# Performance work log

Measured on AMD Instinct MI355X. Metric: run time of the kernel, lower is better.

The kernel has to match this reference:

```python
import jax, jax.numpy as jnp
import numpy as np

DN = ('NCHW', 'OIHW', 'NCHW')

def conv2d(x, w, b, stride, pad):
    y = jax.lax.conv_general_dilated(x, w, (stride, stride), [(pad, pad), (pad, pad)], dimension_numbers=DN)
    return y + b[None, :, None, None]

def conv_transpose2d(x, w, b):
    # torch ConvTranspose2d(k=4, stride=2, padding=1): out = (H-1)*2 - 2 + 4 = 2H
    # implemented as input-dilated conv with padding k-1-p = 2 on each side
    y = jax.lax.conv_general_dilated(x, w, (1, 1), [(2, 2), (2, 2)], lhs_dilation=(2, 2), dimension_numbers=DN)
    return y + b[None, :, None, None]

def setup_inputs() -> dict:
    key = jax.random.key(0)
    ks = jax.random.split(key, 8)
    K, D = 512, 128
    x = jax.random.normal(ks[0], (32, 3, 128, 128), jnp.float32)
    ew1 = jax.random.normal(ks[1], (128, 3, 4, 4), jnp.float32) * (1.0 / np.sqrt(3 * 16))
    eb1 = jnp.zeros((128,), jnp.float32)
    ew2 = jax.random.normal(ks[2], (D, 128, 4, 4), jnp.float32) * (1.0 / np.sqrt(128 * 16))
    eb2 = jnp.zeros((D,), jnp.float32)
    E = jax.random.uniform(ks[3], (K, D), jnp.float32, minval=-1.0 / K, maxval=1.0 / K)
    dw1 = jax.random.normal(ks[4], (128, D, 4, 4), jnp.float32) * (1.0 / np.sqrt(D * 16))
    db1 = jnp.zeros((128,), jnp.float32)
    dw2 = jax.random.normal(ks[5], (3, 128, 4, 4), jnp.float32) * (1.0 / np.sqrt(128 * 16))
    db2 = jnp.zeros((3,), jnp.float32)
    return {"x": x, "ew1": ew1, "eb1": eb1, "ew2": ew2, "eb2": eb2, "E": E,
            "dw1": dw1, "db1": db1, "dw2": dw2, "db2": db2}

def reference(x, ew1, eb1, ew2, eb2, E, dw1, db1, dw2, db2):
    # --- encoder: conv stack ---
    h = jax.nn.relu(conv2d(x, ew1, eb1, stride=2, pad=1))       # [B,128,64,64]
    z = conv2d(h, ew2, eb2, stride=2, pad=1)                    # [B,D,32,32] encoder_output
    B, C, H, W = z.shape
    Ze = jnp.transpose(z, (0, 2, 3, 1)).reshape(-1, C)          # [N_e, D], BHWC flattening
    # --- VQ: pairwise sq-dist, argmin, codebook lookup (== one-hot matmul in original) ---
    d = (jnp.sum(Ze * Ze, axis=1, keepdims=True)
         + jnp.sum(E * E, axis=1)
         - 2.0 * jnp.matmul(Ze, E.T))                           # [N_e, K]
    idx = jnp.argmin(d, axis=1)                                 # [N_e]
    Zq = E[idx]                                                 # [N_e, D]
    # faithful to original: Zq_mat.view(encoder_output.shape) with NO permute back
    dec_in = Zq.reshape(B, C, H, W)
    # straight-through estimator
    dec_in = z + jax.lax.stop_gradient(dec_in - z)
    # --- decoder: transposed conv stack ---
    g = jax.nn.relu(conv_transpose2d(dec_in, dw1, db1))         # [B,128,64,64]
    x_recon = jax.nn.sigmoid(conv_transpose2d(g, dw2, db2))     # [B,3,128,128]
    return x_recon
```

## Files before the change

kernel.cpp:

```cpp
#include <hip/hip_runtime.h>
#include <hip/hip_bf16.h>
#include <math.h>


typedef __attribute__((ext_vector_type(8))) short bf16x8;
typedef __attribute__((ext_vector_type(4))) float f32x4;

__device__ __forceinline__ void gload16(const void* g, const void* l) {
    __builtin_amdgcn_global_load_lds(
        (const __attribute__((address_space(1))) void*)g,
        (__attribute__((address_space(3))) void*)l, 16, 0, 0);
}

__device__ __forceinline__ int fragoff(int row, int ks, int lane) {
    return (row << 8) + (((ks << 6) + (lane & 0x30)) ^ ((row & 7) << 4));
}
__device__ __forceinline__ int fragoff64(int row, int ks, int lane) {
    return (row << 7) + (((ks << 6) + (lane & 0x30)) ^ ((row & 7) << 4));
}

__global__ __launch_bounds__(256) void k_init(
    const float* __restrict__ ew1, const float* __restrict__ ew2,
    const float* __restrict__ E,   const float* __restrict__ dw1,
    const float* __restrict__ dw2,
    __hip_bfloat16* __restrict__ hb,  __hip_bfloat16* __restrict__ w2p,
    __hip_bfloat16* __restrict__ w1p, __hip_bfloat16* __restrict__ Ep,
    __hip_bfloat16* __restrict__ w1b, __hip_bfloat16* __restrict__ w2db9,
    __hip_bfloat16* __restrict__ dq,  float* __restrict__ s2)
{
    int bid = blockIdx.x, t = threadIdx.x;
    if (bid < 4160) {
        int tid = bid * 256 + t;
        const int NROW = 32 * 2 * 66 * 128;
        if (tid < NROW) {
            int c = tid & 127;
            int xx = (tid >> 7) % 66;
            int r2 = tid / (66 * 128);
            int yy = (r2 & 1) * 65;
            int n = r2 >> 1;
            hb[((n * 66 + yy) * 66 + xx) * 128 + c] = __float2bfloat16(0.f);
        } else {
            int t2 = tid - NROW;
            int c = t2 & 127;
            int xs = (t2 >> 7) & 1;
            int yy = ((t2 >> 8) & 63) + 1;
            int n = t2 >> 14;
            hb[((n * 66 + yy) * 66 + xs * 65) * 128 + c] = __float2bfloat16(0.f);
        }
    } else if (bid < 5184) {
        int tid = (bid - 4160) * 256 + t;
        int c = tid & 127, o = (tid >> 7) & 127, rs = tid >> 14;
        int r = rs >> 2, s = rs & 3;
        w2p[tid] = __float2bfloat16(ew2[((o * 128 + c) * 4 + r) * 4 + s]);
    } else if (bid < 6208) {
        int tid = (bid - 5184) * 256 + t;
        int c = tid & 127, o = (tid >> 7) & 127, m = tid >> 14;
        int pe = (m >> 3) & 1, qe = (m >> 2) & 1, tt = (m >> 1) & 1, u = m & 1;
        w1p[tid] = __float2bfloat16(dw1[((o * 128 + c) * 4 + (pe + 2 * tt)) * 4 + (qe + 2 * u)]);
    } else if (bid < 6464) {
        int tid = (bid - 6208) * 256 + t;
        Ep[tid] = __float2bfloat16(E[tid]);
    } else if (bid < 6496) {
        int tid = (bid - 6464) * 256 + t;
        int o = tid >> 6, cpos = tid & 63;
        int slot = cpos >> 3, e = cpos & 7;
        int k = ((slot ^ (o & 7)) << 3) | e;
        float v = 0.f;
        if (k < 48) {
            int c = k >> 4, r = (k >> 2) & 3, s = k & 3;
            v = ew1[((o * 3 + c) * 4 + r) * 4 + s];
        }
        w1b[tid] = __float2bfloat16(v);
    } else if (bid < 6568) {
        int tid = (bid - 6496) * 256 + t;
        int c = tid & 127;
        int col = (tid >> 7) & 15;
        int de = tid >> 11;
        int o = col & 3, pq = col >> 2;
        int d = de / 3, e_ = de - d * 3;
        int pe = pq >> 1, qe = pq & 1;
        int tt = d - pe, u = e_ - qe;
        float v = 0.f;
        if (o < 3 && tt >= 0 && tt < 2 && u >= 0 && u < 2)
            v = dw2[((o * 128 + c) * 4 + (pe + 2 * tt)) * 4 + (qe + 2 * u)];
        w2db9[tid] = __float2bfloat16(v);
    } else if (bid < 6570) {
        int k = (bid - 6568) * 256 + t;
        float a = 0.f;
        const float* e = E + k * 128;
        for (int c = 0; c < 128; ++c) a = fmaf(e[c], e[c], a);
        s2[k] = a;
    } else {
        int tid = (bid - 6570) * 256 + t;
        int n = tid / 16896;
        int rem = tid - n * 16896;
        int c = rem & 127;
        int pp = rem >> 7;
        int yy, xx;
        if (pp < 68) { yy = (pp >= 34) ? 33 : 0; xx = pp % 34; }
        else { int q = pp - 68; yy = 1 + (q >> 1); xx = (q & 1) * 33; }
        dq[((n * 34 + yy) * 34 + xx) * 128 + c] = __float2bfloat16(0.f);
    }
}

__global__ __launch_bounds__(256) void k_conv1g(
    const float* __restrict__ x, const __hip_bfloat16* __restrict__ w1b,
    const float* __restrict__ b1, __hip_bfloat16* __restrict__ hb)
{
    __shared__ char smem[41984];
    int t = threadIdx.x, lane = t & 63, w = t >> 6;
    int wr = w >> 1, wc = w & 1;
    int bid0 = blockIdx.x;
    int bid = ((bid0 & 7) << 7) | (bid0 >> 3);
    int posbase = bid << 7;
    int ng = posbase >> 12, p0g = (posbase >> 6) & 63;

    #pragma unroll
    for (int i = 0; i < 4; ++i)
        gload16(w1b + ((w * 4 + i) * 512 + lane * 8), &smem[16384 + ((w * 4 + i) << 10)]);

    #pragma unroll
    for (int k3 = 0; k3 < 3; ++k3) {
        int j = w + (k3 << 2);
        if (j < 9) {
            int wrow = (j << 1) | (lane >> 5);
            int c = wrow / 6, yy = wrow - c * 6;
            int y = 2 * p0g - 1 + yy;
            int ysrc = y < 0 ? 0 : (y > 127 ? 127 : y);
            gload16(x + (((ng * 3 + c) * 128 + ysrc) << 7) + ((lane & 31) << 2),
                    &smem[32768 + (j << 10)]);
        }
    }
    __syncthreads();

    {
        int row = t >> 1, half = t & 1;
        int pl = row >> 6, q = row & 63;
        #pragma unroll
        for (int j = 0; j < 4; ++j) {
            int d = half * 4 + j;
            int sct = d ^ (row & 7);
            __hip_bfloat16 hv[8];
            #pragma unroll
            for (int e = 0; e < 8; ++e) {
                int k = sct * 8 + e;
                float v = 0.f;
                if (k < 48) {
                    int c = k >> 4, r = (k >> 2) & 3, s4 = k & 3;
                    int y = 2 * (p0g + pl) + r - 1;
                    int xg = 2 * q + s4 - 1;
                    if (((unsigned)y < 128u) && ((unsigned)xg < 128u)) {
                        int wrow = c * 6 + 2 * pl + r;
                        v = *(const float*)&smem[32768 + (wrow << 9) + (xg << 2)];
                    }
                }
                hv[e] = __float2bfloat16(v);
            }
            *(bf16x8*)&smem[(row << 7) + d * 16] = *(bf16x8*)hv;
        }
    }
    __syncthreads();

    f32x4 acc[4][4];
    #pragma unroll
    for (int mi = 0; mi < 4; ++mi)
        #pragma unroll
        for (int ni = 0; ni < 4; ++ni) acc[mi][ni] = (f32x4){0.f, 0.f, 0.f, 0.f};

    #pragma unroll
    for (int ks = 0; ks < 2; ++ks) {
        bf16x8 av[4], bv[4];
        #pragma unroll
        for (int mi = 0; mi < 4; ++mi)
            av[mi] = *(const bf16x8*)&smem[fragoff64((wr << 6) + (mi << 4) + (lane & 15), ks, lane)];
        #pragma unroll
        for (int ni = 0; ni < 4; ++ni)
            bv[ni] = *(const bf16x8*)&smem[16384 + fragoff64((wc << 6) + (ni << 4) + (lane & 15), ks, lane)];
        #pragma unroll
        for (int mi = 0; mi < 4; ++mi)
            #pragma unroll
            for (int ni = 0; ni < 4; ++ni)
                acc[mi][ni] = __builtin_amdgcn_mfma_f32_16x16x32_bf16(av[mi], bv[ni], acc[mi][ni], 0, 0, 0);
    }

    int rg = (lane >> 4) << 2;
    #pragma unroll
    for (int mi = 0; mi < 4; ++mi)
        #pragma unroll
        for (int ni = 0; ni < 4; ++ni) {
            int o = (wc << 6) + (ni << 4) + (lane & 15);
            float bias = b1[o];
            #pragma unroll
            for (int j = 0; j < 4; ++j) {
                int rowg = posbase + (wr << 6) + (mi << 4) + rg + j;
                int n = rowg >> 12, p = (rowg >> 6) & 63, q = rowg & 63;
                float v = acc[mi][ni][j] + bias;
                v = v > 0.f ? v : 0.f;
                hb[((n * 66 + p + 1) * 66 + q + 1) * 128 + o] = __float2bfloat16(v);
            }
        }
}

__global__ __launch_bounds__(256) void k_conv2vq(
    const __hip_bfloat16* __restrict__ hb, const __hip_bfloat16* __restrict__ w2p,
    const float* __restrict__ b2, const __hip_bfloat16* __restrict__ Ep,
    const float* __restrict__ s2, __hip_bfloat16* __restrict__ dq)
{
    __shared__ char smem[49152];
    int t = threadIdx.x, lane = t & 63, w = t >> 6;
    int bid0 = blockIdx.x;
    int bid = ((bid0 & 7) << 6) | (bid0 >> 3);
    int posbase = bid << 6;
    int n = posbase >> 10, p0 = (posbase >> 5) & 31;

    int aoff[2];
    #pragma unroll
    for (int i = 0; i < 2; ++i) {
        int r = ((w << 1) + i) * 8 + (lane >> 3);
        int slot = lane & 7;
        int p = p0 + (r >> 5), q = r & 31;
        aoff[i] = (((n * 66 + 2 * p) * 66 + 2 * q) << 7) + ((slot ^ (r & 7)) << 3);
    }
    int boff[4];
    #pragma unroll
    for (int i = 0; i < 4; ++i) {
        int o = ((w << 2) + i) * 8 + (lane >> 3);
        int slot = lane & 7;
        boff[i] = (o << 7) + ((slot ^ (o & 7)) << 3);
    }

#define C2_STAGE(STEP, BASE) { \
    int rs_ = (STEP) >> 1, ch_ = (STEP) & 1; \
    int aadd_ = ((((rs_ >> 2) * 66) + (rs_ & 3)) << 7) + (ch_ << 6); \
    int badd_ = (rs_ << 14) + (ch_ << 6); \
    _Pragma("unroll") \
    for (int i = 0; i < 2; ++i) \
        gload16(hb + aoff[i] + aadd_, &smem[(BASE) + (((w << 1) + i) << 10)]); \
    _Pragma("unroll") \
    for (int i = 0; i < 4; ++i) \
        gload16(w2p + boff[i] + badd_, &smem[(BASE) + 8192 + (((w << 2) + i) << 10)]); }

    f32x4 acc[4][2];
    #pragma unroll
    for (int mi = 0; mi < 4; ++mi)
        #pragma unroll
        for (int ni = 0; ni < 2; ++ni) acc[mi][ni] = (f32x4){0.f, 0.f, 0.f, 0.f};

    C2_STAGE(0, 0);
    __syncthreads();
    for (int step = 0; step < 32; ++step) {
        int cb = (step & 1) * 24576;
        if (step < 31) C2_STAGE(step + 1, ((step + 1) & 1) * 24576);
        #pragma unroll
        for (int ks = 0; ks < 2; ++ks) {
            bf16x8 av[4], bv[2];
            #pragma unroll
            for (int mi = 0; mi < 4; ++mi)
                av[mi] = *(const bf16x8*)&smem[cb + fragoff64((mi << 4) + (lane & 15), ks, lane)];
            #pragma unroll
            for (int ni = 0; ni < 2; ++ni)
                bv[ni] = *(const bf16x8*)&smem[cb + 8192 + fragoff64((w << 5) + (ni << 4) + (lane & 15), ks, lane)];
            #pragma unroll
            for (int mi = 0; mi < 4; ++mi)
                #pragma unroll
                for (int ni = 0; ni < 2; ++ni)
                    acc[mi][ni] = __builtin_amdgcn_mfma_f32_16x16x32_bf16(av[mi], bv[ni], acc[mi][ni], 0, 0, 0);
        }
        __syncthreads();
    }

#define VQ_STAGE(CHUNK, BASE) { \
    _Pragma("unroll") \
    for (int i = 0; i < 4; ++i) { \
        int kl_ = (((w << 2) + i) << 2) + (lane >> 4); \
        gload16(Ep + ((((CHUNK) << 6) + kl_) << 7) + (((lane & 15) ^ (kl_ & 7)) << 3), \
                &smem[(BASE) + (((w << 2) + i) << 10)]); \
    } }

    {
        int rg = (lane >> 4) << 2;
        #pragma unroll
        for (int mi = 0; mi < 4; ++mi)
            #pragma unroll
            for (int ni = 0; ni < 2; ++ni) {
                int o = (w << 5) + (ni << 4) + (lane & 15);
                float bias = b2[o];
                #pragma unroll
                for (int j = 0; j < 4; ++j) {
                    int r = (mi << 4) + rg + j;
                    int byteoff = (r << 8) + (((((o >> 3) ^ (r & 7))) << 4) | ((o & 7) << 1));
                    __hip_bfloat16 hv = __float2bfloat16(acc[mi][ni][j] + bias);
                    *(__hip_bfloat16*)&smem[byteoff] = hv;
                }
            }
    }
    VQ_STAGE(0, 16384);
    __syncthreads();

    float bvv[4][4];
    int   bii[4][4];
    #pragma unroll
    for (int mi = 0; mi < 4; ++mi)
        #pragma unroll
        for (int j = 0; j < 4; ++j) { bvv[mi][j] = 3.4e38f; bii[mi][j] = 0; }

    for (int chunk = 0; chunk < 8; ++chunk) {
        int eb = 16384 + ((chunk & 1) << 14);
        if (chunk < 7) VQ_STAGE(chunk + 1, 16384 + (((chunk + 1) & 1) << 14));
        f32x4 a2[4];
        #pragma unroll
        for (int mi = 0; mi < 4; ++mi) a2[mi] = (f32x4){0.f, 0.f, 0.f, 0.f};
        #pragma unroll
        for (int ks = 0; ks < 4; ++ks) {
            bf16x8 av[4], bv;
            #pragma unroll
            for (int mi = 0; mi < 4; ++mi)
                av[mi] = *(const bf16x8*)&smem[fragoff((mi << 4) + (lane & 15), ks, lane)];
            bv = *(const bf16x8*)&smem[eb + fragoff((w << 4) + (lane & 15), ks, lane)];
            #pragma unroll
            for (int mi = 0; mi < 4; ++mi)
                a2[mi] = __builtin_amdgcn_mfma_f32_16x16x32_bf16(av[mi], bv, a2[mi], 0, 0, 0);
        }
        int kg = (chunk << 6) + (w << 4) + (lane & 15);
        float s2v = s2[kg];
        #pragma unroll
        for (int mi = 0; mi < 4; ++mi)
            #pragma unroll
            for (int j = 0; j < 4; ++j) {
                float sc = s2v - 2.f * a2[mi][j];
                if (sc < bvv[mi][j]) { bvv[mi][j] = sc; bii[mi][j] = kg; }
            }
        __syncthreads();
    }

    float* redv  = (float*)&smem[16384];
    int*   redi  = (int*)&smem[16384 + 1024];
    int*   idx_l = (int*)&smem[16384 + 2048];
    #pragma unroll
    for (int mi = 0; mi < 4; ++mi)
        #pragma unroll
        for (int j = 0; j < 4; ++j) {
            float v = bvv[mi][j];
            int   ix = bii[mi][j];
            #pragma unroll
            for (int m = 1; m < 16; m <<= 1) {
                float ov = __shfl_xor(v, m, 64);
                int   oi = __shfl_xor(ix, m, 64);
                if (ov < v || (ov == v && oi < ix)) { v = ov; ix = oi; }
            }
            if ((lane & 15) == 0) {
                int r = (mi << 4) + ((lane >> 4) << 2) + j;
                redv[(r << 2) + w] = v;
                redi[(r << 2) + w] = ix;
            }
        }
    __syncthreads();
    if (t < 64) {
        float bv_ = redv[t << 2];
        int   bi_ = redi[t << 2];
        #pragma unroll
        for (int w2 = 1; w2 < 4; ++w2) {
            float ov = redv[(t << 2) + w2];
            int   oi = redi[(t << 2) + w2];
            if (ov < bv_ || (ov == bv_ && oi < bi_)) { bv_ = ov; bi_ = oi; }
        }
        idx_l[t] = bi_;
    }
    __syncthreads();

    #pragma unroll
    for (int i = 0; i < 4; ++i) {
        int idx2 = (w << 2) + i;
        int r = (idx2 << 2) + (lane >> 4);
        int krow = idx_l[r];
        gload16(Ep + ((krow << 7) + ((lane & 15) << 3)), &smem[idx2 << 10]);
    }
    __syncthreads();

    int cd0 = (posbase >> 3) & 127;
    const unsigned short* eb2p = (const unsigned short*)smem;
    #pragma unroll
    for (int k2 = 0; k2 < 4; ++k2) {
        int sp = (k2 << 8) + t;
        int hi = sp >> 7, lo = sp & 127;
        int y = sp >> 5, xx = sp & 31;
        unsigned short vals[8];
        #pragma unroll
        for (int ci = 0; ci < 8; ++ci)
            vals[ci] = eb2p[(((ci << 3) + hi) << 7) + lo];
        __hip_bfloat16* dst = dq + ((n * 34 + y + 1) * 34 + (xx + 1)) * 128 + cd0;
        *(bf16x8*)dst = *(bf16x8*)vals;
    }
}

__global__ __launch_bounds__(256) void k_deconv1(
    const __hip_bfloat16* __restrict__ dq, const __hip_bfloat16* __restrict__ w1p,
    const float* __restrict__ b1, __hip_bfloat16* __restrict__ g)
{
    __shared__ char smem[65536];
    int t = threadIdx.x, lane = t & 63, w = t >> 6;
    int wr = w >> 1, wc = w & 1;
    int bid0 = blockIdx.x;
    int bid = ((bid0 & 7) << 7) | (bid0 >> 3);
    int ag = bid & 7, qe = (bid >> 3) & 1, pe = (bid >> 4) & 1, n = bid >> 5;

    int aoff[4], boff[4];
    #pragma unroll
    for (int i = 0; i < 4; ++i) {
        int r = ((w << 2) + i) * 8 + (lane >> 3);
        int slot = lane & 7;
        int a = (ag << 2) + (r >> 5), b = r & 31;
        aoff[i] = (((n * 34 + (a + pe)) * 34 + (b + qe)) << 7) + ((slot ^ (r & 7)) << 3);
        boff[i] = (r << 7) + ((slot ^ (r & 7)) << 3);
    }
    int mbase = (pe << 3) | (qe << 2);

#define D1_STAGE(STEP, BASE) { \
    int tu_ = (STEP) >> 1, ch_ = (STEP) & 1; \
    int tt_ = tu_ >> 1, u_ = tu_ & 1; \
    int aadd_ = ((tt_ * 34 + u_) << 7) + (ch_ << 6); \
    int badd_ = ((mbase + tu_) << 14) + (ch_ << 6); \
    _Pragma("unroll") \
    for (int i = 0; i < 4; ++i) { \
        gload16(dq + aoff[i] + aadd_, &smem[(BASE) + (((w << 2) + i) << 10)]); \
        gload16(w1p + boff[i] + badd_, &smem[(BASE) + 16384 + (((w << 2) + i) << 10)]); \
    } }

    f32x4 acc[4][4];
    #pragma unroll
    for (int mi = 0; mi < 4; ++mi)
        #pragma unroll
        for (int ni = 0; ni < 4; ++ni) acc[mi][ni] = (f32x4){0.f, 0.f, 0.f, 0.f};

    D1_STAGE(0, 0);
    __syncthreads();
    for (int step = 0; step < 8; ++step) {
        int cb = (step & 1) * 32768;
        if (step < 7) D1_STAGE(step + 1, ((step + 1) & 1) * 32768);
        #pragma unroll
        for (int ks = 0; ks < 2; ++ks) {
            bf16x8 av[4], bv[4];
            #pragma unroll
            for (int mi = 0; mi < 4; ++mi)
                av[mi] = *(const bf16x8*)&smem[cb + fragoff64((wr << 6) + (mi << 4) + (lane & 15), ks, lane)];
            #pragma unroll
            for (int ni = 0; ni < 4; ++ni)
                bv[ni] = *(const bf16x8*)&smem[cb + 16384 + fragoff64((wc << 6) + (ni << 4) + (lane & 15), ks, lane)];
            #pragma unroll
            for (int mi = 0; mi < 4; ++mi)
                #pragma unroll
                for (int ni = 0; ni < 4; ++ni)
                    acc[mi][ni] = __builtin_amdgcn_mfma_f32_16x16x32_bf16(av[mi], bv[ni], acc[mi][ni], 0, 0, 0);
        }
        __syncthreads();
    }

    int rg = (lane >> 4) << 2;
    #pragma unroll
    for (int mi = 0; mi < 4; ++mi)
        #pragma unroll
        for (int ni = 0; ni < 4; ++ni) {
            int o = (wc << 6) + (ni << 4) + (lane & 15);
            float bias = b1[o];
            #pragma unroll
            for (int j = 0; j < 4; ++j) {
                int row = (wr << 6) + (mi << 4) + rg + j;
                int a = (ag << 2) + (row >> 5), b = row & 31;
                int y = 2 * a + pe, xx2 = 2 * b + qe;
                float v = acc[mi][ni][j] + bias;
                v = v > 0.f ? v : 0.f;
                g[((n * 66 + y + 1) * 66 + xx2 + 1) * 128 + o] = __float2bfloat16(v);
            }
        }
}

__global__ __launch_bounds__(256) void k_deconv2g(
    const __hip_bfloat16* __restrict__ g, const __hip_bfloat16* __restrict__ w2db9,
    const float* __restrict__ b2, float* __restrict__ out)
{
    __shared__ char smem[36864];
    int t = threadIdx.x, lane = t & 63, w = t >> 6;
    int bid0 = blockIdx.x;
    int bid = ((bid0 & 7) << 7) | (bid0 >> 3);
    int atile = bid & 31, n = bid >> 5;
    int a0 = atile << 1;

    int aoff[4];
    #pragma unroll
    for (int i = 0; i < 4; ++i) {
        int r = ((w << 2) + i) * 8 + (lane >> 3);
        int al = r >> 6, b = r & 63;
        aoff[i] = (((n * 66 + (a0 + al)) * 66 + b) << 7) + (((lane & 7) ^ (r & 7)) << 3);
    }

#define D2_STAGE(STEP, BASE) { \
    int de_ = (STEP) >> 1, ch_ = (STEP) & 1; \
    int dy_ = de_ / 3, dx_ = de_ - dy_ * 3; \
    int aadd_ = ((dy_ * 66 + dx_) << 7) + (ch_ << 6); \
    _Pragma("unroll") \
    for (int i = 0; i < 4; ++i) \
        gload16(g + aoff[i] + aadd_, &smem[(BASE) + (((w << 2) + i) << 10)]); \
    if (w < 2) { \
        int kl_ = (w << 3) + (lane >> 3); \
        gload16(w2db9 + (de_ << 11) + (kl_ << 7) + (ch_ << 6) + (((lane & 7) ^ (kl_ & 7)) << 3), \
                &smem[(BASE) + 16384 + (w << 10)]); \
    } }

    f32x4 acc[2];
    acc[0] = (f32x4){0.f, 0.f, 0.f, 0.f};
    acc[1] = (f32x4){0.f, 0.f, 0.f, 0.f};

    D2_STAGE(0, 0);
    __syncthreads();
    for (int step = 0; step < 18; ++step) {
        int cb = (step & 1) * 18432;
        if (step < 17) D2_STAGE(step + 1, ((step + 1) & 1) * 18432);
        #pragma unroll
        for (int ks = 0; ks < 2; ++ks) {
            bf16x8 av[2], bv;
            #pragma unroll
            for (int mi = 0; mi < 2; ++mi)
                av[mi] = *(const bf16x8*)&smem[cb + fragoff64((w << 5) + (mi << 4) + (lane & 15), ks, lane)];
            bv = *(const bf16x8*)&smem[cb + 16384 + fragoff64(lane & 15, ks, lane)];
            #pragma unroll
            for (int mi = 0; mi < 2; ++mi)
                acc[mi] = __builtin_amdgcn_mfma_f32_16x16x32_bf16(av[mi], bv, acc[mi], 0, 0, 0);
        }
        __syncthreads();
    }

    int rg = (lane >> 4) << 2;
    int col = lane & 15, o = col & 3, pq = col >> 2;
    if (o < 3) {
        int pe = pq >> 1, qe = pq & 1;
        float bias = b2[o];
        #pragma unroll
        for (int mi = 0; mi < 2; ++mi)
            #pragma unroll
            for (int j = 0; j < 4; ++j) {
                int row = (w << 5) + (mi << 4) + rg + j;
                int y = 2 * (a0 + (row >> 6)) + pe;
                int x = 2 * (row & 63) + qe;
                float v = acc[mi][j] + bias;
                out[((n * 3 + o) * 128 + y) * 128 + x] = 1.f / (1.f + expf(-v));
            }
    }
}

extern "C" void kernel_launch(void* const* d_in, const int* in_sizes, int n_in,
                              void* d_out, int out_size, void* d_ws, size_t ws_size,
                              hipStream_t stream) {
    const float* x   = (const float*)d_in[0];
    const float* ew1 = (const float*)d_in[1];
    const float* eb1 = (const float*)d_in[2];
    const float* ew2 = (const float*)d_in[3];
    const float* eb2 = (const float*)d_in[4];
    const float* E   = (const float*)d_in[5];
    const float* dw1 = (const float*)d_in[6];
    const float* db1 = (const float*)d_in[7];
    const float* dw2 = (const float*)d_in[8];
    const float* db2 = (const float*)d_in[9];
    float* out = (float*)d_out;

    char* W = (char*)d_ws;
    __hip_bfloat16* hb    = (__hip_bfloat16*)(W + 0);
    __hip_bfloat16* g     = (__hip_bfloat16*)(W + 0);
    __hip_bfloat16* dq    = (__hip_bfloat16*)(W + 75497472);
    __hip_bfloat16* w2p   = (__hip_bfloat16*)(W + 84967424);
    __hip_bfloat16* w1p   = (__hip_bfloat16*)(W + 85491712);
    __hip_bfloat16* Ep    = (__hip_bfloat16*)(W + 86016000);
    __hip_bfloat16* w2db9 = (__hip_bfloat16*)(W + 86147072);
    float*          s2    = (float*)(W + 86184192);
    __hip_bfloat16* w1b   = (__hip_bfloat16*)(W + 86186240);

    k_init    <<<8682, 256, 0, stream>>>(ew1, ew2, E, dw1, dw2,
                                         hb, w2p, w1p, Ep, w1b, w2db9, dq, s2);
    k_conv1g  <<<1024, 256, 0, stream>>>(x, w1b, eb1, hb);
    k_conv2vq <<<512,  256, 0, stream>>>(hb, w2p, eb2, Ep, s2, dq);
    k_deconv1 <<<1024, 256, 0, stream>>>(dq, w1p, db1, g);
    k_deconv2g<<<1024, 256, 0, stream>>>(g, w2db9, db2, out);
}
```

Measured before the change: 112.5 us.

## Deepen LDS pipelines with smaller K-chunks and waitcnt barriers in conv kernels

Reworks the main GEMM loops of conv2, deconv1 and deconv2 to stage 32-element K chunks instead of 64, using 3–4 rotating LDS buffers with a new XOR swizzle. Each iteration now uses a single s_waitcnt vmcnt(N) plus barrier instead of a full __syncthreads, so several global-to-LDS loads stay in flight while MFMAs run. The goal is to hide global load latency and to shrink LDS footprint for higher occupancy. The cost is more loop iterations and barriers, and correctness now depends on the hand-written vmcnt counts matching the number of loads issued per stage.

```diff
diff --git a/kernel.cpp b/kernel.cpp
--- a/kernel.cpp
+++ b/kernel.cpp
@@ -12,8 +12,13 @@
         (__attribute__((address_space(3))) void*)l, 16, 0, 0);
 }
 
+#define WAITBAR(N) asm volatile("s_waitcnt vmcnt(" #N ")\n\ts_barrier" ::: "memory")
+
 __device__ __forceinline__ int fragoff(int row, int ks, int lane) {
     return (row << 8) + (((ks << 6) + (lane & 0x30)) ^ ((row & 7) << 4));
+}
+__device__ __forceinline__ int fragoff32(int row, int lane) {
+    return (row << 6) + ((((lane >> 4) ^ ((row >> 1) & 3))) << 4);
 }
 __device__ __forceinline__ int fragoff64(int row, int ks, int lane) {
     return (row << 7) + (((ks << 6) + (lane & 0x30)) ^ ((row & 7) << 4));
@@ -213,32 +218,27 @@
     int posbase = bid << 6;
     int n = posbase >> 10, p0 = (posbase >> 5) & 31;
 
-    int aoff[2];
+    int aoffA;
+    {
+        int r = (w << 4) + (lane >> 2), d = lane & 3;
+        int p = p0 + (r >> 5), q = r & 31;
+        aoffA = (((n * 66 + 2 * p) * 66 + 2 * q) << 7) + ((d ^ ((r >> 1) & 3)) << 3);
+    }
+    int boff[2];
     #pragma unroll
     for (int i = 0; i < 2; ++i) {
-        int r = ((w << 1) + i) * 8 + (lane >> 3);
-        int slot = lane & 7;
-        int p = p0 + (r >> 5), q = r & 31;
-        aoff[i] = (((n * 66 + 2 * p) * 66 + 2 * q) << 7) + ((slot ^ (r & 7)) << 3);
-    }
-    int boff[4];
-    #pragma unroll
-    for (int i = 0; i < 4; ++i) {
-        int o = ((w << 2) + i) * 8 + (lane >> 3);
-        int slot = lane & 7;
-        boff[i] = (o << 7) + ((slot ^ (o & 7)) << 3);
+        int r = ((w << 1) + i) * 16 + (lane >> 2), d = lane & 3;
+        boff[i] = (r << 7) + ((d ^ ((r >> 1) & 3)) << 3);
     }
 
 #define C2_STAGE(STEP, BASE) { \
-    int rs_ = (STEP) >> 1, ch_ = (STEP) & 1; \
-    int aadd_ = ((((rs_ >> 2) * 66) + (rs_ & 3)) << 7) + (ch_ << 6); \
-    int badd_ = (rs_ << 14) + (ch_ << 6); \
+    int rs_ = (STEP) >> 2, q_ = (STEP) & 3; \
+    int aadd_ = ((((rs_ >> 2) * 66) + (rs_ & 3)) << 7) + (q_ << 5); \
+    int badd_ = (rs_ << 14) + (q_ << 5); \
+    gload16(hb + aoffA + aadd_, &smem[(BASE) + (w << 10)]); \
     _Pragma("unroll") \
     for (int i = 0; i < 2; ++i) \
-        gload16(hb + aoff[i] + aadd_, &smem[(BASE) + (((w << 1) + i) << 10)]); \
-    _Pragma("unroll") \
-    for (int i = 0; i < 4; ++i) \
-        gload16(w2p + boff[i] + badd_, &smem[(BASE) + 8192 + (((w << 2) + i) << 10)]); }
+        gload16(w2p + boff[i] + badd_, &smem[(BASE) + 4096 + (((w << 1) + i) << 10)]); }
 
     f32x4 acc[4][2];
     #pragma unroll
@@ -246,28 +246,30 @@
         #pragma unroll
         for (int ni = 0; ni < 2; ++ni) acc[mi][ni] = (f32x4){0.f, 0.f, 0.f, 0.f};
 
-    C2_STAGE(0, 0);
-    __syncthreads();
-    for (int step = 0; step < 32; ++step) {
-        int cb = (step & 1) * 24576;
-        if (step < 31) C2_STAGE(step + 1, ((step + 1) & 1) * 24576);
-        #pragma unroll
-        for (int ks = 0; ks < 2; ++ks) {
-            bf16x8 av[4], bv[2];
-            #pragma unroll
-            for (int mi = 0; mi < 4; ++mi)
-                av[mi] = *(const bf16x8*)&smem[cb + fragoff64((mi << 4) + (lane & 15), ks, lane)];
+    auto comp = [&](int cb) {
+        bf16x8 av[4], bv[2];
+        #pragma unroll
+        for (int mi = 0; mi < 4; ++mi)
+            av[mi] = *(const bf16x8*)&smem[cb + fragoff32((mi << 4) + (lane & 15), lane)];
+        #pragma unroll
+        for (int ni = 0; ni < 2; ++ni)
+            bv[ni] = *(const bf16x8*)&smem[cb + 4096 + fragoff32((w << 5) + (ni << 4) + (lane & 15), lane)];
+        #pragma unroll
+        for (int mi = 0; mi < 4; ++mi)
             #pragma unroll
             for (int ni = 0; ni < 2; ++ni)
-                bv[ni] = *(const bf16x8*)&smem[cb + 8192 + fragoff64((w << 5) + (ni << 4) + (lane & 15), ks, lane)];
-            #pragma unroll
-            for (int mi = 0; mi < 4; ++mi)
-                #pragma unroll
-                for (int ni = 0; ni < 2; ++ni)
-                    acc[mi][ni] = __builtin_amdgcn_mfma_f32_16x16x32_bf16(av[mi], bv[ni], acc[mi][ni], 0, 0, 0);
-        }
-        __syncthreads();
-    }
+                acc[mi][ni] = __builtin_amdgcn_mfma_f32_16x16x32_bf16(av[mi], bv[ni], acc[mi][ni], 0, 0, 0);
+    };
+
+    C2_STAGE(0, 0); C2_STAGE(1, 12288); C2_STAGE(2, 24576);
+    for (int st = 0; st < 62; ++st) {
+        WAITBAR(6);
+        if (st + 3 < 64) C2_STAGE(st + 3, ((st + 3) & 3) * 12288);
+        comp((st & 3) * 12288);
+    }
+    WAITBAR(3); comp((62 & 3) * 12288);
+    WAITBAR(0); comp((63 & 3) * 12288);
+    __syncthreads();
 
 #define VQ_STAGE(CHUNK, BASE) { \
     _Pragma("unroll") \
@@ -397,33 +399,33 @@
     const __hip_bfloat16* __restrict__ dq, const __hip_bfloat16* __restrict__ w1p,
     const float* __restrict__ b1, __hip_bfloat16* __restrict__ g)
 {
-    __shared__ char smem[65536];
+    __shared__ char smem[49152];
     int t = threadIdx.x, lane = t & 63, w = t >> 6;
     int wr = w >> 1, wc = w & 1;
     int bid0 = blockIdx.x;
     int bid = ((bid0 & 7) << 7) | (bid0 >> 3);
     int ag = bid & 7, qe = (bid >> 3) & 1, pe = (bid >> 4) & 1, n = bid >> 5;
 
-    int aoff[4], boff[4];
-    #pragma unroll
-    for (int i = 0; i < 4; ++i) {
-        int r = ((w << 2) + i) * 8 + (lane >> 3);
-        int slot = lane & 7;
+    int aoff[2], boff[2];
+    #pragma unroll
+    for (int i = 0; i < 2; ++i) {
+        int r = ((w << 1) + i) * 16 + (lane >> 2), d = lane & 3;
         int a = (ag << 2) + (r >> 5), b = r & 31;
-        aoff[i] = (((n * 34 + (a + pe)) * 34 + (b + qe)) << 7) + ((slot ^ (r & 7)) << 3);
-        boff[i] = (r << 7) + ((slot ^ (r & 7)) << 3);
+        int csw = (d ^ ((r >> 1) & 3)) << 3;
+        aoff[i] = (((n * 34 + (a + pe)) * 34 + (b + qe)) << 7) + csw;
+        boff[i] = (r << 7) + csw;
     }
     int mbase = (pe << 3) | (qe << 2);
 
 #define D1_STAGE(STEP, BASE) { \
-    int tu_ = (STEP) >> 1, ch_ = (STEP) & 1; \
+    int tu_ = (STEP) >> 2, q_ = (STEP) & 3; \
     int tt_ = tu_ >> 1, u_ = tu_ & 1; \
-    int aadd_ = ((tt_ * 34 + u_) << 7) + (ch_ << 6); \
-    int badd_ = ((mbase + tu_) << 14) + (ch_ << 6); \
+    int aadd_ = ((tt_ * 34 + u_) << 7) + (q_ << 5); \
+    int badd_ = ((mbase + tu_) << 14) + (q_ << 5); \
     _Pragma("unroll") \
-    for (int i = 0; i < 4; ++i) { \
-        gload16(dq + aoff[i] + aadd_, &smem[(BASE) + (((w << 2) + i) << 10)]); \
-        gload16(w1p + boff[i] + badd_, &smem[(BASE) + 16384 + (((w << 2) + i) << 10)]); \
+    for (int i = 0; i < 2; ++i) { \
+        gload16(dq + aoff[i] + aadd_, &smem[(BASE) + (((w << 1) + i) << 10)]); \
+        gload16(w1p + boff[i] + badd_, &smem[(BASE) + 8192 + (((w << 1) + i) << 10)]); \
     } }
 
     f32x4 acc[4][4];
@@ -432,28 +434,28 @@
         #pragma unroll
         for (int ni = 0; ni < 4; ++ni) acc[mi][ni] = (f32x4){0.f, 0.f, 0.f, 0.f};
 
-    D1_STAGE(0, 0);
-    __syncthreads();
-    for (int step = 0; step < 8; ++step) {
-        int cb = (step & 1) * 32768;
-        if (step < 7) D1_STAGE(step + 1, ((step + 1) & 1) * 32768);
-        #pragma unroll
-        for (int ks = 0; ks < 2; ++ks) {
-            bf16x8 av[4], bv[4];
-            #pragma unroll
-            for (int mi = 0; mi < 4; ++mi)
-                av[mi] = *(const bf16x8*)&smem[cb + fragoff64((wr << 6) + (mi << 4) + (lane & 15), ks, lane)];
+    auto comp = [&](int cb) {
+        bf16x8 av[4], bv[4];
+        #pragma unroll
+        for (int mi = 0; mi < 4; ++mi)
+            av[mi] = *(const bf16x8*)&smem[cb + fragoff32((wr << 6) + (mi << 4) + (lane & 15), lane)];
+        #pragma unroll
+        for (int ni = 0; ni < 4; ++ni)
+            bv[ni] = *(const bf16x8*)&smem[cb + 8192 + fragoff32((wc << 6) + (ni << 4) + (lane & 15), lane)];
+        #pragma unroll
+        for (int mi = 0; mi < 4; ++mi)
             #pragma unroll
             for (int ni = 0; ni < 4; ++ni)
-                bv[ni] = *(const bf16x8*)&smem[cb + 16384 + fragoff64((wc << 6) + (ni << 4) + (lane & 15), ks, lane)];
-            #pragma unroll
-            for (int mi = 0; mi < 4; ++mi)
-                #pragma unroll
-                for (int ni = 0; ni < 4; ++ni)
-                    acc[mi][ni] = __builtin_amdgcn_mfma_f32_16x16x32_bf16(av[mi], bv[ni], acc[mi][ni], 0, 0, 0);
-        }
-        __syncthreads();
-    }
+                acc[mi][ni] = __builtin_amdgcn_mfma_f32_16x16x32_bf16(av[mi], bv[ni], acc[mi][ni], 0, 0, 0);
+    };
+
+    D1_STAGE(0, 0); D1_STAGE(1, 16384);
+    for (int st = 0; st < 15; ++st) {
+        WAITBAR(4);
+        if (st + 2 < 16) D1_STAGE(st + 2, ((st + 2) % 3) * 16384);
+        comp((st % 3) * 16384);
+    }
+    WAITBAR(0); comp((15 % 3) * 16384);
 
     int rg = (lane >> 4) << 2;
     #pragma unroll
@@ -478,56 +480,57 @@
     const __hip_bfloat16* __restrict__ g, const __hip_bfloat16* __restrict__ w2db9,
     const float* __restrict__ b2, float* __restrict__ out)
 {
-    __shared__ char smem[36864];
+    __shared__ char smem[27648];
     int t = threadIdx.x, lane = t & 63, w = t >> 6;
     int bid0 = blockIdx.x;
     int bid = ((bid0 & 7) << 7) | (bid0 >> 3);
     int atile = bid & 31, n = bid >> 5;
     int a0 = atile << 1;
 
-    int aoff[4];
-    #pragma unroll
-    for (int i = 0; i < 4; ++i) {
-        int r = ((w << 2) + i) * 8 + (lane >> 3);
+    int aoff[2];
+    #pragma unroll
+    for (int i = 0; i < 2; ++i) {
+        int r = ((w << 1) + i) * 16 + (lane >> 2), d = lane & 3;
         int al = r >> 6, b = r & 63;
-        aoff[i] = (((n * 66 + (a0 + al)) * 66 + b) << 7) + (((lane & 7) ^ (r & 7)) << 3);
+        aoff[i] = (((n * 66 + (a0 + al)) * 66 + b) << 7) + ((d ^ ((r >> 1) & 3)) << 3);
+    }
+    int boffB;
+    {
+        int r = lane >> 2, d = lane & 3;
+        boffB = (r << 7) + ((d ^ ((r >> 1) & 3)) << 3);
     }
 
 #define D2_STAGE(STEP, BASE) { \
-    int de_ = (STEP) >> 1, ch_ = (STEP) & 1; \
+    int de_ = (STEP) >> 2, q_ = (STEP) & 3; \
     int dy_ = de_ / 3, dx_ = de_ - dy_ * 3; \
-    int aadd_ = ((dy_ * 66 + dx_) << 7) + (ch_ << 6); \
+    int aadd_ = ((dy_ * 66 + dx_) << 7) + (q_ << 5); \
     _Pragma("unroll") \
-    for (int i = 0; i < 4; ++i) \
-        gload16(g + aoff[i] + aadd_, &smem[(BASE) + (((w << 2) + i) << 10)]); \
-    if (w < 2) { \
-        int kl_ = (w << 3) + (lane >> 3); \
-        gload16(w2db9 + (de_ << 11) + (kl_ << 7) + (ch_ << 6) + (((lane & 7) ^ (kl_ & 7)) << 3), \
-                &smem[(BASE) + 16384 + (w << 10)]); \
-    } }
+    for (int i = 0; i < 2; ++i) \
+        gload16(g + aoff[i] + aadd_, &smem[(BASE) + (((w << 1) + i) << 10)]); \
+    gload16(w2db9 + (de_ << 11) + boffB + (q_ << 5), &smem[(BASE) + 8192]); }
 
     f32x4 acc[2];
     acc[0] = (f32x4){0.f, 0.f, 0.f, 0.f};
     acc[1] = (f32x4){0.f, 0.f, 0.f, 0.f};
 
-    D2_STAGE(0, 0);
-    __syncthreads();
-    for (int step = 0; step < 18; ++step) {
-        int cb = (step & 1) * 18432;
-        if (step < 17) D2_STAGE(step + 1, ((step + 1) & 1) * 18432);
-        #pragma unroll
-        for (int ks = 0; ks < 2; ++ks) {
-            bf16x8 av[2], bv;
-            #pragma unroll
-            for (int mi = 0; mi < 2; ++mi)
-                av[mi] = *(const bf16x8*)&smem[cb + fragoff64((w << 5) + (mi << 4) + (lane & 15), ks, lane)];
-            bv = *(const bf16x8*)&smem[cb + 16384 + fragoff64(lane & 15, ks, lane)];
-            #pragma unroll
-            for (int mi = 0; mi < 2; ++mi)
-                acc[mi] = __builtin_amdgcn_mfma_f32_16x16x32_bf16(av[mi], bv, acc[mi], 0, 0, 0);
-        }
-        __syncthreads();
-    }
+    auto comp = [&](int cb) {
+        bf16x8 av[2], bv;
+        #pragma unroll
+        for (int mi = 0; mi < 2; ++mi)
+            av[mi] = *(const bf16x8*)&smem[cb + fragoff32((w << 5) + (mi << 4) + (lane & 15), lane)];
+        bv = *(const bf16x8*)&smem[cb + 8192 + fragoff32(lane & 15, lane)];
+        #pragma unroll
+        for (int mi = 0; mi < 2; ++mi)
+            acc[mi] = __builtin_amdgcn_mfma_f32_16x16x32_bf16(av[mi], bv, acc[mi], 0, 0, 0);
+    };
+
+    D2_STAGE(0, 0); D2_STAGE(1, 9216);
+    for (int st = 0; st < 35; ++st) {
+        WAITBAR(3);
+        if (st + 2 < 36) D2_STAGE(st + 2, ((st + 2) % 3) * 9216);
+        comp((st % 3) * 9216);
+    }
+    WAITBAR(0); comp((35 % 3) * 9216);
 
     int rg = (lane >> 4) << 2;
     int col = lane & 15, o = col & 3, pq = col >> 2;
```

Result: slower. 121.8 us (+8.2%).

## Double conv2+VQ block tile to 128 positions with 2x2 warp layout

Applied to the files above, without the earlier changes.

The fused conv2+VQ kernel now gives each block 128 output positions instead of 64. Warps are arranged 2x2, each owning a 64x64 accumulator tile, so A and B tiles are reused across more MFMAs. The grid drops from 512 to 256 blocks and shared memory grows to 64KB. The aim is to halve repeated weight and codebook loads per position, at the cost of lower occupancy, more register pressure, and only 256 blocks to spread across the CUs.

```diff
diff --git a/kernel.cpp b/kernel.cpp
--- a/kernel.cpp
+++ b/kernel.cpp
@@ -206,27 +206,23 @@
     const float* __restrict__ b2, const __hip_bfloat16* __restrict__ Ep,
     const float* __restrict__ s2, __hip_bfloat16* __restrict__ dq)
 {
-    __shared__ char smem[49152];
+    __shared__ char smem[65536];
     int t = threadIdx.x, lane = t & 63, w = t >> 6;
+    int wr = w >> 1, wc = w & 1;
     int bid0 = blockIdx.x;
-    int bid = ((bid0 & 7) << 6) | (bid0 >> 3);
-    int posbase = bid << 6;
+    int bid = ((bid0 & 7) << 5) | (bid0 >> 3);
+    int posbase = bid << 7;
     int n = posbase >> 10, p0 = (posbase >> 5) & 31;
 
-    int aoff[2];
-    #pragma unroll
-    for (int i = 0; i < 2; ++i) {
-        int r = ((w << 1) + i) * 8 + (lane >> 3);
+    int aoff[4], boff[4];
+    #pragma unroll
+    for (int i = 0; i < 4; ++i) {
+        int r = ((w << 2) + i) * 8 + (lane >> 3);
         int slot = lane & 7;
         int p = p0 + (r >> 5), q = r & 31;
-        aoff[i] = (((n * 66 + 2 * p) * 66 + 2 * q) << 7) + ((slot ^ (r & 7)) << 3);
-    }
-    int boff[4];
-    #pragma unroll
-    for (int i = 0; i < 4; ++i) {
-        int o = ((w << 2) + i) * 8 + (lane >> 3);
-        int slot = lane & 7;
-        boff[i] = (o << 7) + ((slot ^ (o & 7)) << 3);
+        int csw = (slot ^ (r & 7)) << 3;
+        aoff[i] = (((n * 66 + 2 * p) * 66 + 2 * q) << 7) + csw;
+        boff[i] = (r << 7) + csw;
     }
 
 #define C2_STAGE(STEP, BASE) { \
@@ -234,36 +230,35 @@
     int aadd_ = ((((rs_ >> 2) * 66) + (rs_ & 3)) << 7) + (ch_ << 6); \
     int badd_ = (rs_ << 14) + (ch_ << 6); \
     _Pragma("unroll") \
-    for (int i = 0; i < 2; ++i) \
-        gload16(hb + aoff[i] + aadd_, &smem[(BASE) + (((w << 1) + i) << 10)]); \
-    _Pragma("unroll") \
-    for (int i = 0; i < 4; ++i) \
-        gload16(w2p + boff[i] + badd_, &smem[(BASE) + 8192 + (((w << 2) + i) << 10)]); }
-
-    f32x4 acc[4][2];
+    for (int i = 0; i < 4; ++i) { \
+        gload16(hb + aoff[i] + aadd_, &smem[(BASE) + (((w << 2) + i) << 10)]); \
+        gload16(w2p + boff[i] + badd_, &smem[(BASE) + 16384 + (((w << 2) + i) << 10)]); \
+    } }
+
+    f32x4 acc[4][4];
     #pragma unroll
     for (int mi = 0; mi < 4; ++mi)
         #pragma unroll
-        for (int ni = 0; ni < 2; ++ni) acc[mi][ni] = (f32x4){0.f, 0.f, 0.f, 0.f};
+        for (int ni = 0; ni < 4; ++ni) acc[mi][ni] = (f32x4){0.f, 0.f, 0.f, 0.f};
 
     C2_STAGE(0, 0);
     __syncthreads();
     for (int step = 0; step < 32; ++step) {
-        int cb = (step & 1) * 24576;
-        if (step < 31) C2_STAGE(step + 1, ((step + 1) & 1) * 24576);
+        int cb = (step & 1) * 32768;
+        if (step < 31) C2_STAGE(step + 1, ((step + 1) & 1) * 32768);
         #pragma unroll
         for (int ks = 0; ks < 2; ++ks) {
-            bf16x8 av[4], bv[2];
+            bf16x8 av[4], bv[4];
             #pragma unroll
             for (int mi = 0; mi < 4; ++mi)
-                av[mi] = *(const bf16x8*)&smem[cb + fragoff64((mi << 4) + (lane & 15), ks, lane)];
-            #pragma unroll
-            for (int ni = 0; ni < 2; ++ni)
-                bv[ni] = *(const bf16x8*)&smem[cb + 8192 + fragoff64((w << 5) + (ni << 4) + (lane & 15), ks, lane)];
+                av[mi] = *(const bf16x8*)&smem[cb + fragoff64((wr << 6) + (mi << 4) + (lane & 15), ks, lane)];
+            #pragma unroll
+            for (int ni = 0; ni < 4; ++ni)
+                bv[ni] = *(const bf16x8*)&smem[cb + 16384 + fragoff64((wc << 6) + (ni << 4) + (lane & 15), ks, lane)];
             #pragma unroll
             for (int mi = 0; mi < 4; ++mi)
                 #pragma unroll
-                for (int ni = 0; ni < 2; ++ni)
+                for (int ni = 0; ni < 4; ++ni)
                     acc[mi][ni] = __builtin_amdgcn_mfma_f32_16x16x32_bf16(av[mi], bv[ni], acc[mi][ni], 0, 0, 0);
         }
         __syncthreads();
@@ -282,49 +277,47 @@
         #pragma unroll
         for (int mi = 0; mi < 4; ++mi)
             #pragma unroll
-            for (int ni = 0; ni < 2; ++ni) {
-                int o = (w << 5) + (ni << 4) + (lane & 15);
+            for (int ni = 0; ni < 4; ++ni) {
+                int o = (wc << 6) + (ni << 4) + (lane & 15);
                 float bias = b2[o];
                 #pragma unroll
                 for (int j = 0; j < 4; ++j) {
-                    int r = (mi << 4) + rg + j;
+                    int r = (wr << 6) + (mi << 4) + rg + j;
                     int byteoff = (r << 8) + (((((o >> 3) ^ (r & 7))) << 4) | ((o & 7) << 1));
                     __hip_bfloat16 hv = __float2bfloat16(acc[mi][ni][j] + bias);
                     *(__hip_bfloat16*)&smem[byteoff] = hv;
                 }
             }
     }
-    VQ_STAGE(0, 16384);
-    __syncthreads();
-
-    float bvv[4][4];
-    int   bii[4][4];
-    #pragma unroll
-    for (int mi = 0; mi < 4; ++mi)
+    VQ_STAGE(0, 32768);
+    __syncthreads();
+
+    float bvv[8][4];
+    int   bii[8][4];
+    #pragma unroll
+    for (int mi = 0; mi < 8; ++mi)
         #pragma unroll
         for (int j = 0; j < 4; ++j) { bvv[mi][j] = 3.4e38f; bii[mi][j] = 0; }
 
     for (int chunk = 0; chunk < 8; ++chunk) {
-        int eb = 16384 + ((chunk & 1) << 14);
-        if (chunk < 7) VQ_STAGE(chunk + 1, 16384 + (((chunk + 1) & 1) << 14));
-        f32x4 a2[4];
-        #pragma unroll
-        for (int mi = 0; mi < 4; ++mi) a2[mi] = (f32x4){0.f, 0.f, 0.f, 0.f};
+        int eb = 32768 + ((chunk & 1) << 14);
+        if (chunk < 7) VQ_STAGE(chunk + 1, 32768 + (((chunk + 1) & 1) << 14));
+        f32x4 a2[8];
+        #pragma unroll
+        for (int mi = 0; mi < 8; ++mi) a2[mi] = (f32x4){0.f, 0.f, 0.f, 0.f};
         #pragma unroll
         for (int ks = 0; ks < 4; ++ks) {
-            bf16x8 av[4], bv;
-            #pragma unroll
-            for (int mi = 0; mi < 4; ++mi)
-                av[mi] = *(const bf16x8*)&smem[fragoff((mi << 4) + (lane & 15), ks, lane)];
-            bv = *(const bf16x8*)&smem[eb + fragoff((w << 4) + (lane & 15), ks, lane)];
-            #pragma unroll
-            for (int mi = 0; mi < 4; ++mi)
-                a2[mi] = __builtin_amdgcn_mfma_f32_16x16x32_bf16(av[mi], bv, a2[mi], 0, 0, 0);
+            bf16x8 bv = *(const bf16x8*)&smem[eb + fragoff((w << 4) + (lane & 15), ks, lane)];
+            #pragma unroll
+            for (int mi = 0; mi < 8; ++mi) {
+                bf16x8 av = *(const bf16x8*)&smem[fragoff((mi << 4) + (lane & 15), ks, lane)];
+                a2[mi] = __builtin_amdgcn_mfma_f32_16x16x32_bf16(av, bv, a2[mi], 0, 0, 0);
+            }
         }
         int kg = (chunk << 6) + (w << 4) + (lane & 15);
         float s2v = s2[kg];
         #pragma unroll
-        for (int mi = 0; mi < 4; ++mi)
+        for (int mi = 0; mi < 8; ++mi)
             #pragma unroll
             for (int j = 0; j < 4; ++j) {
                 float sc = s2v - 2.f * a2[mi][j];
@@ -333,11 +326,11 @@
         __syncthreads();
     }
 
-    float* redv  = (float*)&smem[16384];
-    int*   redi  = (int*)&smem[16384 + 1024];
-    int*   idx_l = (int*)&smem[16384 + 2048];
-    #pragma unroll
-    for (int mi = 0; mi < 4; ++mi)
+    float* redv  = (float*)&smem[32768];
+    int*   redi  = (int*)&smem[32768 + 2048];
+    int*   idx_l = (int*)&smem[32768 + 4096];
+    #pragma unroll
+    for (int mi = 0; mi < 8; ++mi)
         #pragma unroll
         for (int j = 0; j < 4; ++j) {
             float v = bvv[mi][j];
@@ -355,7 +348,7 @@
             }
         }
     __syncthreads();
-    if (t < 64) {
+    if (t < 128) {
         float bv_ = redv[t << 2];
         int   bi_ = redi[t << 2];
         #pragma unroll
@@ -369,8 +362,8 @@
     __syncthreads();
 
     #pragma unroll
-    for (int i = 0; i < 4; ++i) {
-        int idx2 = (w << 2) + i;
+    for (int i = 0; i < 8; ++i) {
+        int idx2 = (w << 3) + i;
         int r = (idx2 << 2) + (lane >> 4);
         int krow = idx_l[r];
         gload16(Ep + ((krow << 7) + ((lane & 15) << 3)), &smem[idx2 << 10]);
@@ -383,13 +376,14 @@
     for (int k2 = 0; k2 < 4; ++k2) {
         int sp = (k2 << 8) + t;
         int hi = sp >> 7, lo = sp & 127;
-        int y = sp >> 5, xx = sp & 31;
-        unsigned short vals[8];
-        #pragma unroll
-        for (int ci = 0; ci < 8; ++ci)
-            vals[ci] = eb2p[(((ci << 3) + hi) << 7) + lo];
+        int y = hi * 4 + (lo >> 5), xx = lo & 31;
+        unsigned short vals[16];
+        #pragma unroll
+        for (int ci = 0; ci < 16; ++ci)
+            vals[ci] = eb2p[(((ci << 3) | hi) << 7) + lo];
         __hip_bfloat16* dst = dq + ((n * 34 + y + 1) * 34 + (xx + 1)) * 128 + cd0;
-        *(bf16x8*)dst = *(bf16x8*)vals;
+        *(bf16x8*)dst = *(bf16x8*)&vals[0];
+        *(bf16x8*)(dst + 8) = *(bf16x8*)&vals[8];
     }
 }
 
@@ -576,7 +570,7 @@
     k_init    <<<8682, 256, 0, stream>>>(ew1, ew2, E, dw1, dw2,
                                          hb, w2p, w1p, Ep, w1b, w2db9, dq, s2);
     k_conv1g  <<<1024, 256, 0, stream>>>(x, w1b, eb1, hb);
-    k_conv2vq <<<512,  256, 0, stream>>>(hb, w2p, eb2, Ep, s2, dq);
+    k_conv2vq <<<256,  256, 0, stream>>>(hb, w2p, eb2, Ep, s2, dq);
     k_deconv1 <<<1024, 256, 0, stream>>>(dq, w1p, db1, g);
     k_deconv2g<<<1024, 256, 0, stream>>>(g, w2db9, db2, out);
 }
```

Measured after the change: 128.9 us. 14.5% more time.
